# Kernel optimization log

Measured on AMD Instinct MI355X. Metric: run time of the kernel, lower is better.

Reference implementation:

```python
import jax, jax.numpy as jnp
import numpy as np

D_MODEL = 1024
D_INNER = 2048   # expand_factor * d_model
D_STATE = 16
D_CONV = 4
DT_RANK = 64     # ceil(d_model / 16)
EPS = 1e-5


def setup_inputs() -> dict:
    key = jax.random.key(0)
    ks = jax.random.split(key, 10)
    B, L = 2, 1024
    w = lambda k, shape, s: (jax.random.normal(k, shape, jnp.float32) * s)
    A = jnp.tile(jnp.arange(1, D_STATE + 1, dtype=jnp.float32), (D_INNER, 1))
    return {
        "hidden_states": jax.random.normal(ks[0], (B, L, D_MODEL), jnp.float32),
        "norm_w": jnp.ones((D_MODEL,), jnp.float32),
        "norm_b": jnp.zeros((D_MODEL,), jnp.float32),
        "in_proj_w": w(ks[1], (D_MODEL, 2 * D_INNER), 0.02),
        "conv_w": w(ks[2], (D_INNER, D_CONV), 0.2),
        "conv_b": jnp.zeros((D_INNER,), jnp.float32),
        "x_proj_w": w(ks[3], (D_INNER, DT_RANK + 2 * D_STATE), 0.02),
        "dt_proj_w": w(ks[4], (DT_RANK, D_INNER), 0.1),
        "dt_proj_b": w(ks[5], (D_INNER,), 0.1),
        "A_log": jnp.log(A),
        "D_param": jnp.ones((D_INNER,), jnp.float32),
        "out_proj_w": w(ks[6], (D_INNER, D_MODEL), 0.02),
    }


def _causal_depthwise_conv(x, conv_w, conv_b):
    # x: [B, L, d_inner] -> causal depthwise conv, kernel size D_CONV
    B, L, C = x.shape
    xt = jnp.transpose(x, (0, 2, 1))                 # [B, C, L]
    xt = jnp.pad(xt, ((0, 0), (0, 0), (D_CONV - 1, 0)))  # left pad == torch pad+truncate
    k = conv_w[:, None, :]                            # [C, 1, K] (OIH, groups=C)
    y = jax.lax.conv_general_dilated(
        xt, k, window_strides=(1,), padding="VALID",
        dimension_numbers=("NCH", "OIH", "NCH"), feature_group_count=C)
    y = y + conv_b[None, :, None]
    return jnp.transpose(y, (0, 2, 1))                # [B, L, C]


def _selective_scan(u, delta, A, Bm, Cm, D_param):
    # u, delta: [B, L, d_inner]; A: [d_inner, d_state]; Bm, Cm: [B, L, d_state]
    dA = jnp.exp(delta[..., None] * A[None, None])            # [B,L,d,n]
    dBu = delta[..., None] * Bm[:, :, None, :] * u[..., None]  # [B,L,d,n]
    h0 = jnp.zeros((u.shape[0], u.shape[2], A.shape[1]), u.dtype)

    def step(h, inp):
        dA_t, dBu_t, c_t = inp          # [B,d,n], [B,d,n], [B,n]
        h = dA_t * h + dBu_t
        y = jnp.einsum("bdn,bn->bd", h, c_t)
        return h, y

    xs = (jnp.moveaxis(dA, 1, 0), jnp.moveaxis(dBu, 1, 0), jnp.moveaxis(Cm, 1, 0))
    _, ys = jax.lax.scan(step, h0, xs)   # ys: [L, B, d]
    y = jnp.moveaxis(ys, 0, 1)           # [B, L, d]
    return y + u * D_param[None, None]


def reference(hidden_states, norm_w, norm_b, in_proj_w, conv_w, conv_b,
              x_proj_w, dt_proj_w, dt_proj_b, A_log, D_param, out_proj_w):
    h = hidden_states
    mu = jnp.mean(h, axis=-1, keepdims=True)
    var = jnp.mean(jnp.square(h - mu), axis=-1, keepdims=True)
    h = (h - mu) * jax.lax.rsqrt(var + EPS) * norm_w + norm_b

    xz = h @ in_proj_w                       # [B,L,2*d_inner]
    x, z = jnp.split(xz, 2, axis=-1)
    x = _causal_depthwise_conv(x, conv_w, conv_b)
    x = jax.nn.silu(x)

    A = -jnp.exp(A_log)                      # [d_inner, d_state]
    xp = x @ x_proj_w                        # [B,L,dt_rank+2*d_state]
    dt_r = xp[..., :DT_RANK]
    Bm = xp[..., DT_RANK:DT_RANK + D_STATE]
    Cm = xp[..., DT_RANK + D_STATE:]
    delta = jax.nn.softplus(dt_r @ dt_proj_w + dt_proj_b)  # [B,L,d_inner]

    y = _selective_scan(x, delta, A, Bm, Cm, D_param)
    y = y * jax.nn.silu(z)
    return y @ out_proj_w
```

## Files before the change

### kernel.cpp

```cpp
#include <hip/hip_runtime.h>
#include <hip/hip_bf16.h>

#define D_MODEL 1024
#define D_INNER 2048
#define D_STATE 16
#define DT_RANK 64
#define NB 2
#define LSEQ 1024
#define NROWS (NB * LSEQ)
#define XPN 96
#define NC 32
#define CL 32

typedef __attribute__((ext_vector_type(8))) short bf16x8;
typedef __attribute__((ext_vector_type(4))) float f32x4;

__device__ __forceinline__ unsigned short f2bf(float x) {
    __hip_bfloat16 h = __float2bfloat16(x);
    return *reinterpret_cast<unsigned short*>(&h);
}
__device__ __forceinline__ float bf2f(unsigned short u) {
    unsigned int v = ((unsigned int)u) << 16;
    float f;
    __builtin_memcpy(&f, &v, 4);
    return f;
}
__device__ __forceinline__ unsigned short f2h(float x) {
    _Float16 h = (_Float16)x;
    unsigned short u;
    __builtin_memcpy(&u, &h, 2);
    return u;
}
__device__ __forceinline__ float h2f(unsigned short u) {
    _Float16 h;
    __builtin_memcpy(&h, &u, 2);
    return (float)h;
}

__global__ __launch_bounds__(256) void ln_kernel(const float* __restrict__ x,
                                                 const float* __restrict__ w,
                                                 const float* __restrict__ bnorm,
                                                 unsigned short* __restrict__ outb) {
    int row = blockIdx.x;
    const float4* xr = (const float4*)(x + (size_t)row * D_MODEL);
    float4 v = xr[threadIdx.x];
    float s = v.x + v.y + v.z + v.w;
    float sq = v.x * v.x + v.y * v.y + v.z * v.z + v.w * v.w;
#pragma unroll
    for (int off = 32; off > 0; off >>= 1) {
        s += __shfl_down(s, off);
        sq += __shfl_down(sq, off);
    }
    __shared__ float ws[4], wq[4];
    __shared__ float smu, srstd;
    int wave = threadIdx.x >> 6;
    if ((threadIdx.x & 63) == 0) { ws[wave] = s; wq[wave] = sq; }
    __syncthreads();
    if (threadIdx.x == 0) {
        float ts = ws[0] + ws[1] + ws[2] + ws[3];
        float tq = wq[0] + wq[1] + wq[2] + wq[3];
        float mu = ts * (1.f / D_MODEL);
        float var = tq * (1.f / D_MODEL) - mu * mu;
        smu = mu;
        srstd = rsqrtf(var + 1e-5f);
    }
    __syncthreads();
    float mu = smu, rstd = srstd;
    float4 wv = ((const float4*)w)[threadIdx.x];
    float4 bv = ((const float4*)bnorm)[threadIdx.x];
    ushort4 pk;
    pk.x = f2bf((v.x - mu) * rstd * wv.x + bv.x);
    pk.y = f2bf((v.y - mu) * rstd * wv.y + bv.y);
    pk.z = f2bf((v.z - mu) * rstd * wv.z + bv.z);
    pk.w = f2bf((v.w - mu) * rstd * wv.w + bv.w);
    *(ushort4*)(outb + (size_t)row * D_MODEL + threadIdx.x * 4) = pk;
}

__global__ __launch_bounds__(256) void wcast_t(const float* __restrict__ W,
                                               unsigned short* __restrict__ Wt,
                                               int K, int Nreal, int Npad) {
    __shared__ float t[32][33];
    int tn = blockIdx.x * 32, tk = blockIdx.y * 32;
    for (int e = threadIdx.x; e < 1024; e += 256) {
        int r = e >> 5, c = e & 31;
        int n = tn + c;
        t[r][c] = (n < Nreal) ? W[(size_t)(tk + r) * Nreal + n] : 0.f;
    }
    __syncthreads();
    for (int e = threadIdx.x; e < 1024; e += 256) {
        int r = e >> 5, c = e & 31;
        Wt[(size_t)(tn + r) * K + tk + c] = f2bf(t[c][r]);
    }
}

template <int EPI>
__global__ __launch_bounds__(256) void gemm_bf16(const unsigned short* __restrict__ A,
                                                 const unsigned short* __restrict__ Bt,
                                                 const float* __restrict__ bias,
                                                 float* __restrict__ C,
                                                 void* __restrict__ C2,
                                                 int M, int K, int ldc, int Nreal) {
    __shared__ unsigned short As[128 * 32];
    __shared__ unsigned short Bs[128 * 32];
    int nwg = gridDim.x * gridDim.y;
    int orig = blockIdx.y * gridDim.x + blockIdx.x;
    int q = nwg >> 3, r = nwg & 7;
    int xcd = orig & 7, idx = orig >> 3;
    int newid = (xcd < r ? xcd * (q + 1) : r * (q + 1) + (xcd - r) * q) + idx;
    int bx = newid % gridDim.x, by = newid / gridDim.x;

    int tid = threadIdx.x;
    int lane = tid & 63;
    int wave = tid >> 6;
    int wr = (wave >> 1) * 64, wc = (wave & 1) * 64;
    int bm = by * 128, bn = bx * 128;
    int kchunk = K / gridDim.z;
    int kbeg = blockIdx.z * kchunk;

    f32x4 acc[4][4];
#pragma unroll
    for (int i = 0; i < 4; ++i)
#pragma unroll
        for (int j = 0; j < 4; ++j) acc[i][j] = (f32x4){0.f, 0.f, 0.f, 0.f};

    int r0 = tid >> 2;
    int c0 = (tid & 3) * 8;
    const unsigned short* a0 = A + (size_t)(bm + r0) * K + c0;
    const unsigned short* a1 = A + (size_t)(bm + 64 + r0) * K + c0;
    const unsigned short* b0 = Bt + (size_t)(bn + r0) * K + c0;
    const unsigned short* b1 = Bt + (size_t)(bn + 64 + r0) * K + c0;
    unsigned short* asw0 = As + (size_t)(tid & ~63) * 8;
    unsigned short* asw1 = As + 2048 + (size_t)(tid & ~63) * 8;
    unsigned short* bsw0 = Bs + (size_t)(tid & ~63) * 8;
    unsigned short* bsw1 = Bs + 2048 + (size_t)(tid & ~63) * 8;

    int ar = lane & 15;
    int ko = (lane >> 4) * 8;

    for (int k0 = kbeg; k0 < kbeg + kchunk; k0 += 32) {
        __syncthreads();
        __builtin_amdgcn_global_load_lds((const __attribute__((address_space(1))) void*)(a0 + k0),
                                         (__attribute__((address_space(3))) void*)asw0, 16, 0, 0);
        __builtin_amdgcn_global_load_lds((const __attribute__((address_space(1))) void*)(a1 + k0),
                                         (__attribute__((address_space(3))) void*)asw1, 16, 0, 0);
        __builtin_amdgcn_global_load_lds((const __attribute__((address_space(1))) void*)(b0 + k0),
                                         (__attribute__((address_space(3))) void*)bsw0, 16, 0, 0);
        __builtin_amdgcn_global_load_lds((const __attribute__((address_space(1))) void*)(b1 + k0),
                                         (__attribute__((address_space(3))) void*)bsw1, 16, 0, 0);
        __syncthreads();
        bf16x8 af[4], bfr[4];
#pragma unroll
        for (int i = 0; i < 4; ++i)
            af[i] = *(const bf16x8*)&As[(size_t)(wr + i * 16 + ar) * 32 + ko];
#pragma unroll
        for (int j = 0; j < 4; ++j)
            bfr[j] = *(const bf16x8*)&Bs[(size_t)(wc + j * 16 + ar) * 32 + ko];
#pragma unroll
        for (int i = 0; i < 4; ++i)
#pragma unroll
            for (int j = 0; j < 4; ++j)
                acc[i][j] = __builtin_amdgcn_mfma_f32_16x16x32_bf16(af[i], bfr[j], acc[i][j], 0, 0, 0);
    }

    int crow0 = bm + wr + (lane >> 4) * 4;
    int ccol0 = bn + wc + (lane & 15);
    size_t zoff = (size_t)blockIdx.z * (size_t)M * ldc;
#pragma unroll
    for (int i = 0; i < 4; ++i)
#pragma unroll
        for (int j = 0; j < 4; ++j) {
            int col = ccol0 + j * 16;
            if (EPI == 0) {
                if (col < Nreal) {
                    float* cp = C + zoff + (size_t)(crow0 + i * 16) * ldc + col;
#pragma unroll
                    for (int rr = 0; rr < 4; ++rr) cp[(size_t)rr * ldc] = acc[i][j][rr];
                }
            } else if (EPI == 1) {
                float bv = bias[col];
#pragma unroll
                for (int rr = 0; rr < 4; ++rr) {
                    float v = acc[i][j][rr] + bv;
                    v = (v > 20.f) ? v : log1pf(__expf(v));
                    C[(size_t)(crow0 + i * 16 + rr) * ldc + col] = v;
                }
            } else if (EPI == 2) {
                if (col < 2048) {
#pragma unroll
                    for (int rr = 0; rr < 4; ++rr)
                        C[(size_t)(crow0 + i * 16 + rr) * 2048 + col] = acc[i][j][rr];
                } else {
                    unsigned short* cz = (unsigned short*)C2;
#pragma unroll
                    for (int rr = 0; rr < 4; ++rr)
                        cz[(size_t)(crow0 + i * 16 + rr) * 2048 + (col - 2048)] = f2bf(acc[i][j][rr]);
                }
            } else {
                unsigned short* cp = (unsigned short*)C2 + zoff + (size_t)(crow0 + i * 16) * ldc + col;
#pragma unroll
                for (int rr = 0; rr < 4; ++rr) cp[(size_t)rr * ldc] = f2h(acc[i][j][rr]);
            }
        }
}

__global__ __launch_bounds__(256) void reduce_xp(const float* __restrict__ part,
                                                 float* __restrict__ xp,
                                                 unsigned short* __restrict__ dtr) {
    int t = blockIdx.x * 256 + threadIdx.x;
    float s = 0.f;
#pragma unroll
    for (int k = 0; k < 16; ++k) s += part[(size_t)k * (NROWS * XPN) + t];
    xp[t] = s;
    int row = t / 96, col = t - row * 96;
    if (col < 64) dtr[(size_t)row * 64 + col] = f2bf(s);
}

__global__ __launch_bounds__(256) void reduce_out(const unsigned short* __restrict__ part,
                                                  float* __restrict__ out) {
    int t = blockIdx.x * 256 + threadIdx.x;
    const size_t stride = (size_t)NROWS * D_MODEL;
    ushort4 p0 = ((const ushort4*)part)[t];
    ushort4 p1 = ((const ushort4*)(part + stride))[t];
    ushort4 p2 = ((const ushort4*)(part + 2 * stride))[t];
    ushort4 p3 = ((const ushort4*)(part + 3 * stride))[t];
    float4 o;
    o.x = h2f(p0.x) + h2f(p1.x) + h2f(p2.x) + h2f(p3.x);
    o.y = h2f(p0.y) + h2f(p1.y) + h2f(p2.y) + h2f(p3.y);
    o.z = h2f(p0.z) + h2f(p1.z) + h2f(p2.z) + h2f(p3.z);
    o.w = h2f(p0.w) + h2f(p1.w) + h2f(p2.w) + h2f(p3.w);
    ((float4*)out)[t] = o;
}

__global__ __launch_bounds__(256) void conv_silu_kernel(const float* __restrict__ xx,
                                                        const float* __restrict__ cw,
                                                        const float* __restrict__ cb,
                                                        unsigned short* __restrict__ outb) {
    int gid = blockIdx.x * 256 + threadIdx.x;
    int d4 = (gid & 511) << 2;
    int bl = gid >> 9;
    int l = bl & (LSEQ - 1);
    const float* base = xx + (size_t)bl * D_INNER + d4;
    float4 zr = make_float4(0.f, 0.f, 0.f, 0.f);
    float4 x0 = *(const float4*)base;
    float4 x1 = (l >= 1) ? *(const float4*)(base - D_INNER) : zr;
    float4 x2 = (l >= 2) ? *(const float4*)(base - 2 * D_INNER) : zr;
    float4 x3 = (l >= 3) ? *(const float4*)(base - 3 * D_INNER) : zr;
    float4 bias = *(const float4*)(cb + d4);
    const float4* wv = (const float4*)(cw + (size_t)d4 * 4);
    float xs0[4] = {x0.x, x0.y, x0.z, x0.w};
    float xs1[4] = {x1.x, x1.y, x1.z, x1.w};
    float xs2[4] = {x2.x, x2.y, x2.z, x2.w};
    float xs3[4] = {x3.x, x3.y, x3.z, x3.w};
    float bs[4] = {bias.x, bias.y, bias.z, bias.w};
    ushort4 ob;
    unsigned short* obp = (unsigned short*)&ob;
#pragma unroll
    for (int e = 0; e < 4; ++e) {
        float4 we = wv[e];
        float acc = bs[e];
        acc = fmaf(we.w, xs0[e], acc);
        acc = fmaf(we.z, xs1[e], acc);
        acc = fmaf(we.y, xs2[e], acc);
        acc = fmaf(we.x, xs3[e], acc);
        obp[e] = f2bf(acc / (1.f + __expf(-acc)));
    }
    *(ushort4*)(outb + (size_t)bl * D_INNER + d4) = ob;
}

__global__ __launch_bounds__(256) void scan_local(const float* __restrict__ xp,
                                                  const float* __restrict__ delta,
                                                  const unsigned short* __restrict__ ub,
                                                  const float* __restrict__ A_log,
                                                  float* __restrict__ hst,
                                                  float* __restrict__ sdel) {
    int bc = blockIdx.x >> 3;
    int b = bc >> 5, c = bc & (NC - 1);
    int d = (blockIdx.x & 7) * 256 + threadIdx.x;
    int base_r = b * LSEQ + c * CL;
    __shared__ float Bsm[CL * 16];
    for (int e = threadIdx.x; e < CL * 16; e += 256) {
        int l = e >> 4, n = e & 15;
        Bsm[e] = xp[(size_t)(base_r + l) * XPN + DT_RANK + n];
    }
    __syncthreads();
    float Av[16];
    const float4* ap = (const float4*)(A_log + (size_t)d * 16);
#pragma unroll
    for (int qq = 0; qq < 4; ++qq) {
        float4 a = ap[qq];
        Av[4 * qq + 0] = -__expf(a.x); Av[4 * qq + 1] = -__expf(a.y);
        Av[4 * qq + 2] = -__expf(a.z); Av[4 * qq + 3] = -__expf(a.w);
    }
    float h[16] = {};
    float sd = 0.f;
    const float* dp = delta + (size_t)base_r * D_INNER + d;
    const unsigned short* up = ub + (size_t)base_r * D_INNER + d;
#pragma unroll 4
    for (int l = 0; l < CL; ++l) {
        float dv = dp[(size_t)l * D_INNER];
        float u = bf2f(up[(size_t)l * D_INNER]);
        float du = dv * u;
        sd += dv;
#pragma unroll
        for (int n = 0; n < 16; ++n) {
            float dA = __expf(dv * Av[n]);
            h[n] = fmaf(dA, h[n], du * Bsm[l * 16 + n]);
        }
    }
    size_t hi = ((size_t)(c * NB + b) * D_INNER + d) * 16;
#pragma unroll
    for (int qq = 0; qq < 4; ++qq) {
        float4 v = make_float4(h[4 * qq], h[4 * qq + 1], h[4 * qq + 2], h[4 * qq + 3]);
        *(float4*)(hst + hi + 4 * qq) = v;
    }
    sdel[(size_t)(c * NB + b) * D_INNER + d] = sd;
}

__global__ __launch_bounds__(256) void scan_combine(const float* __restrict__ A_log,
                                                    const float* __restrict__ sdel,
                                                    float* __restrict__ hst) {
    int t = blockIdx.x * 256 + threadIdx.x;
    int n = t & 15, d = (t >> 4) & (D_INNER - 1), b = t >> 15;
    float Avn = -__expf(A_log[(size_t)d * 16 + n]);
    float h = 0.f;
#pragma unroll 4
    for (int c = 0; c < NC; ++c) {
        size_t base = (size_t)(c * NB + b) * D_INNER + d;
        float* hp = hst + base * 16 + n;
        float S = sdel[base];
        float tmp = *hp;
        *hp = h;
        h = fmaf(__expf(Avn * S), h, tmp);
    }
}

__global__ __launch_bounds__(256) void scan_final(const float* __restrict__ xp,
                                                  const float* __restrict__ dlt,
                                                  const unsigned short* __restrict__ ub,
                                                  const unsigned short* __restrict__ zb,
                                                  const float* __restrict__ hst,
                                                  const float* __restrict__ A_log,
                                                  const float* __restrict__ Dp,
                                                  unsigned short* __restrict__ yb) {
    int bc = blockIdx.x >> 3;
    int b = bc >> 5, c = bc & (NC - 1);
    int d = (blockIdx.x & 7) * 256 + threadIdx.x;
    int base_r = b * LSEQ + c * CL;
    __shared__ float Bsm[CL * 16], Csm[CL * 16];
    for (int e = threadIdx.x; e < CL * 16; e += 256) {
        int l = e >> 4, n = e & 15;
        Bsm[e] = xp[(size_t)(base_r + l) * XPN + DT_RANK + n];
        Csm[e] = xp[(size_t)(base_r + l) * XPN + DT_RANK + 16 + n];
    }
    __syncthreads();
    float Av[16];
    const float4* ap = (const float4*)(A_log + (size_t)d * 16);
#pragma unroll
    for (int qq = 0; qq < 4; ++qq) {
        float4 a = ap[qq];
        Av[4 * qq + 0] = -__expf(a.x); Av[4 * qq + 1] = -__expf(a.y);
        Av[4 * qq + 2] = -__expf(a.z); Av[4 * qq + 3] = -__expf(a.w);
    }
    float h[16];
    size_t hi = ((size_t)(c * NB + b) * D_INNER + d) * 16;
#pragma unroll
    for (int qq = 0; qq < 4; ++qq) {
        float4 v = *(const float4*)(hst + hi + 4 * qq);
        h[4 * qq] = v.x; h[4 * qq + 1] = v.y; h[4 * qq + 2] = v.z; h[4 * qq + 3] = v.w;
    }
    float Dv = Dp[d];
    const float* dyp = dlt + (size_t)base_r * D_INNER + d;
    const unsigned short* up = ub + (size_t)base_r * D_INNER + d;
    const unsigned short* zp = zb + (size_t)base_r * D_INNER + d;
#pragma unroll 4
    for (int l = 0; l < CL; ++l) {
        float dv = dyp[(size_t)l * D_INNER];
        float u = bf2f(up[(size_t)l * D_INNER]);
        float du = dv * u;
        float acc = 0.f;
#pragma unroll
        for (int n = 0; n < 16; ++n) {
            float dA = __expf(dv * Av[n]);
            h[n] = fmaf(dA, h[n], du * Bsm[l * 16 + n]);
            acc = fmaf(h[n], Csm[l * 16 + n], acc);
        }
        float yv = fmaf(u, Dv, acc);
        float zv = bf2f(zp[(size_t)l * D_INNER]);
        float sz = zv / (1.f + __expf(-zv));
        yb[(size_t)(base_r + l) * D_INNER + d] = f2bf(yv * sz);
    }
}

extern "C" void kernel_launch(void* const* d_in, const int* in_sizes, int n_in,
                              void* d_out, int out_size, void* d_ws, size_t ws_size,
                              hipStream_t stream) {
    const float* hidden = (const float*)d_in[0];
    const float* norm_w = (const float*)d_in[1];
    const float* norm_b = (const float*)d_in[2];
    const float* in_proj_w = (const float*)d_in[3];
    const float* conv_w = (const float*)d_in[4];
    const float* conv_b = (const float*)d_in[5];
    const float* x_proj_w = (const float*)d_in[6];
    const float* dt_proj_w = (const float*)d_in[7];
    const float* dt_proj_b = (const float*)d_in[8];
    const float* A_log = (const float*)d_in[9];
    const float* D_param = (const float*)d_in[10];
    const float* out_proj_w = (const float*)d_in[11];
    float* out = (float*)d_out;

    float* wsf = (float*)d_ws;
    unsigned short* hbufb = (unsigned short*)wsf;
    float* xpbuf = wsf;
    float* sdelbuf = wsf + 196608;
    unsigned short* dtrb = (unsigned short*)(wsf + 327680);
    unsigned short* wDt = (unsigned short*)(wsf + 458752);
    unsigned short* wOt = (unsigned short*)wsf;
    float* xzx = wsf + 1048576;
    unsigned short* xzz = (unsigned short*)(wsf + 5242880);
    unsigned short* xcb = (unsigned short*)(wsf + 7340032);
    unsigned short* yb = xcb;
    float* dltbuf = wsf + 9437184;
    unsigned short* wAt = (unsigned short*)dltbuf;
    float* xpart = dltbuf;
    unsigned short* wXt = (unsigned short*)(dltbuf + 3145728);
    float* hst = xzx;
    unsigned short* opart = (unsigned short*)xzx;

    wcast_t<<<dim3(4096 / 32, 1024 / 32), 256, 0, stream>>>(in_proj_w, wAt, 1024, 4096, 4096);
    wcast_t<<<dim3(128 / 32, 2048 / 32), 256, 0, stream>>>(x_proj_w, wXt, 2048, 96, 128);

    ln_kernel<<<NROWS, 256, 0, stream>>>(hidden, norm_w, norm_b, hbufb);

    gemm_bf16<2><<<dim3(4096 / 128, NROWS / 128, 1), 256, 0, stream>>>(
        hbufb, wAt, nullptr, xzx, xzz, NROWS, 1024, 2048, 4096);

    wcast_t<<<dim3(2048 / 32, 64 / 32), 256, 0, stream>>>(dt_proj_w, wDt, 64, 2048, 2048);

    conv_silu_kernel<<<(NROWS * D_INNER) / 1024, 256, 0, stream>>>(xzx, conv_w, conv_b, xcb);

    gemm_bf16<0><<<dim3(1, NROWS / 128, 16), 256, 0, stream>>>(
        xcb, wXt, nullptr, xpart, nullptr, NROWS, 2048, XPN, XPN);

    reduce_xp<<<(NROWS * XPN) / 256, 256, 0, stream>>>(xpart, xpbuf, dtrb);

    gemm_bf16<1><<<dim3(D_INNER / 128, NROWS / 128, 1), 256, 0, stream>>>(
        dtrb, wDt, dt_proj_b, dltbuf, nullptr, NROWS, 64, D_INNER, D_INNER);

    scan_local<<<NB * NC * (D_INNER / 256), 256, 0, stream>>>(
        xpbuf, dltbuf, xcb, A_log, hst, sdelbuf);
    scan_combine<<<(NB * D_INNER * D_STATE) / 256, 256, 0, stream>>>(
        A_log, sdelbuf, hst);
    scan_final<<<NB * NC * (D_INNER / 256), 256, 0, stream>>>(
        xpbuf, dltbuf, xcb, xzz, hst, A_log, D_param, yb);

    wcast_t<<<dim3(1024 / 32, 2048 / 32), 256, 0, stream>>>(out_proj_w, wOt, 2048, 1024, 1024);

    gemm_bf16<3><<<dim3(1024 / 128, NROWS / 128, 4), 256, 0, stream>>>(
        yb, wOt, nullptr, nullptr, opart, NROWS, 2048, 1024, 1024);

    reduce_out<<<(NROWS * D_MODEL / 4) / 256, 256, 0, stream>>>(opart, out);
}
```

Measured before the change: 200.6 us.

## Fuse dt_proj into xp reduction, merge weight casts, store x and delta as bf16

The three weight transpose-casts are merged into one launch, and the dt_proj weight cast is dropped. The xp partial-sum reduction now also performs the small dt_proj matmul in fp32 on CUDA cores, followed by the softplus, which removes a separate GEMM launch and the dtr buffer. The x half of in_proj and the delta tensor are stored as bf16 instead of fp32, which cuts memory traffic in the conv, scan_local and scan_final kernels. The cost is lower precision for x and delta, and a per-block CUDA-core matmul that re-reads dt_proj_w from global memory.

```diff
diff --git a/kernel.cpp b/kernel.cpp
--- a/kernel.cpp
+++ b/kernel.cpp
@@ -11,6 +11,7 @@
 #define XPN 96
 #define NC 32
 #define CL 32
+#define DR_ROWS 8
 
 typedef __attribute__((ext_vector_type(8))) short bf16x8;
 typedef __attribute__((ext_vector_type(4))) float f32x4;
@@ -76,11 +77,18 @@
     *(ushort4*)(outb + (size_t)row * D_MODEL + threadIdx.x * 4) = pk;
 }
 
-__global__ __launch_bounds__(256) void wcast_t(const float* __restrict__ W,
-                                               unsigned short* __restrict__ Wt,
-                                               int K, int Nreal, int Npad) {
+__global__ __launch_bounds__(256) void wcast_all(const float* __restrict__ W0, unsigned short* __restrict__ D0,
+                                                 const float* __restrict__ W1, unsigned short* __restrict__ D1,
+                                                 const float* __restrict__ W2, unsigned short* __restrict__ D2) {
+    int bid = blockIdx.x;
+    const float* W;
+    unsigned short* Dst;
+    int K, Nreal, bx, by;
+    if (bid < 4096) { W = W0; Dst = D0; K = 1024; Nreal = 4096; bx = bid & 127; by = bid >> 7; }
+    else if (bid < 4352) { int j = bid - 4096; W = W1; Dst = D1; K = 2048; Nreal = 96; bx = j & 3; by = j >> 2; }
+    else { int j = bid - 4352; W = W2; Dst = D2; K = 2048; Nreal = 1024; bx = j & 31; by = j >> 5; }
     __shared__ float t[32][33];
-    int tn = blockIdx.x * 32, tk = blockIdx.y * 32;
+    int tn = bx * 32, tk = by * 32;
     for (int e = threadIdx.x; e < 1024; e += 256) {
         int r = e >> 5, c = e & 31;
         int n = tn + c;
@@ -89,14 +97,13 @@
     __syncthreads();
     for (int e = threadIdx.x; e < 1024; e += 256) {
         int r = e >> 5, c = e & 31;
-        Wt[(size_t)(tn + r) * K + tk + c] = f2bf(t[c][r]);
+        Dst[(size_t)(tn + r) * K + tk + c] = f2bf(t[c][r]);
     }
 }
 
 template <int EPI>
 __global__ __launch_bounds__(256) void gemm_bf16(const unsigned short* __restrict__ A,
                                                  const unsigned short* __restrict__ Bt,
-                                                 const float* __restrict__ bias,
                                                  float* __restrict__ C,
                                                  void* __restrict__ C2,
                                                  int M, int K, int ldc, int Nreal) {
@@ -176,21 +183,14 @@
 #pragma unroll
                     for (int rr = 0; rr < 4; ++rr) cp[(size_t)rr * ldc] = acc[i][j][rr];
                 }
-            } else if (EPI == 1) {
-                float bv = bias[col];
-#pragma unroll
-                for (int rr = 0; rr < 4; ++rr) {
-                    float v = acc[i][j][rr] + bv;
-                    v = (v > 20.f) ? v : log1pf(__expf(v));
-                    C[(size_t)(crow0 + i * 16 + rr) * ldc + col] = v;
-                }
             } else if (EPI == 2) {
+                unsigned short* cx = (unsigned short*)C;
+                unsigned short* cz = (unsigned short*)C2;
                 if (col < 2048) {
 #pragma unroll
                     for (int rr = 0; rr < 4; ++rr)
-                        C[(size_t)(crow0 + i * 16 + rr) * 2048 + col] = acc[i][j][rr];
+                        cx[(size_t)(crow0 + i * 16 + rr) * 2048 + col] = f2bf(acc[i][j][rr]);
                 } else {
-                    unsigned short* cz = (unsigned short*)C2;
 #pragma unroll
                     for (int rr = 0; rr < 4; ++rr)
                         cz[(size_t)(crow0 + i * 16 + rr) * 2048 + (col - 2048)] = f2bf(acc[i][j][rr]);
@@ -203,16 +203,55 @@
         }
 }
 
-__global__ __launch_bounds__(256) void reduce_xp(const float* __restrict__ part,
-                                                 float* __restrict__ xp,
-                                                 unsigned short* __restrict__ dtr) {
-    int t = blockIdx.x * 256 + threadIdx.x;
-    float s = 0.f;
-#pragma unroll
-    for (int k = 0; k < 16; ++k) s += part[(size_t)k * (NROWS * XPN) + t];
-    xp[t] = s;
-    int row = t / 96, col = t - row * 96;
-    if (col < 64) dtr[(size_t)row * 64 + col] = f2bf(s);
+__global__ __launch_bounds__(256) void reduce_delta(const float* __restrict__ part,
+                                                    const float* __restrict__ Wdt,
+                                                    const float* __restrict__ dtb,
+                                                    float* __restrict__ xp,
+                                                    unsigned short* __restrict__ delta) {
+    int r0 = blockIdx.x * DR_ROWS;
+    __shared__ float dtr[DR_ROWS][64];
+    for (int idx = threadIdx.x; idx < DR_ROWS * XPN; idx += 256) {
+        int rr = idx / XPN, cc = idx - rr * XPN;
+        size_t off = (size_t)(r0 + rr) * XPN + cc;
+        float s = 0.f;
+#pragma unroll
+        for (int p = 0; p < 16; ++p) s += part[(size_t)p * ((size_t)NROWS * XPN) + off];
+        xp[off] = s;
+        if (cc < 64) dtr[rr][cc] = s;
+    }
+    __syncthreads();
+    int c0 = threadIdx.x * 8;
+    float acc[DR_ROWS][8] = {};
+    for (int k = 0; k < 64; ++k) {
+        float4 w0 = *(const float4*)(Wdt + (size_t)k * D_INNER + c0);
+        float4 w1 = *(const float4*)(Wdt + (size_t)k * D_INNER + c0 + 4);
+        float wv[8] = {w0.x, w0.y, w0.z, w0.w, w1.x, w1.y, w1.z, w1.w};
+#pragma unroll
+        for (int rr = 0; rr < DR_ROWS; ++rr) {
+            float s = dtr[rr][k];
+#pragma unroll
+            for (int j = 0; j < 8; ++j) acc[rr][j] = fmaf(s, wv[j], acc[rr][j]);
+        }
+    }
+    float4 b0 = *(const float4*)(dtb + c0);
+    float4 b1 = *(const float4*)(dtb + c0 + 4);
+    float bias[8] = {b0.x, b0.y, b0.z, b0.w, b1.x, b1.y, b1.z, b1.w};
+#pragma unroll
+    for (int rr = 0; rr < DR_ROWS; ++rr) {
+        ushort4 o0, o1;
+        unsigned short tmp[8];
+#pragma unroll
+        for (int j = 0; j < 8; ++j) {
+            float v = acc[rr][j] + bias[j];
+            v = (v > 20.f) ? v : log1pf(__expf(v));
+            tmp[j] = f2bf(v);
+        }
+        o0.x = tmp[0]; o0.y = tmp[1]; o0.z = tmp[2]; o0.w = tmp[3];
+        o1.x = tmp[4]; o1.y = tmp[5]; o1.z = tmp[6]; o1.w = tmp[7];
+        unsigned short* dp = delta + (size_t)(r0 + rr) * D_INNER + c0;
+        *(ushort4*)dp = o0;
+        *(ushort4*)(dp + 4) = o1;
+    }
 }
 
 __global__ __launch_bounds__(256) void reduce_out(const unsigned short* __restrict__ part,
@@ -231,7 +270,7 @@
     ((float4*)out)[t] = o;
 }
 
-__global__ __launch_bounds__(256) void conv_silu_kernel(const float* __restrict__ xx,
+__global__ __launch_bounds__(256) void conv_silu_kernel(const unsigned short* __restrict__ xx,
                                                         const float* __restrict__ cw,
                                                         const float* __restrict__ cb,
                                                         unsigned short* __restrict__ outb) {
@@ -239,18 +278,18 @@
     int d4 = (gid & 511) << 2;
     int bl = gid >> 9;
     int l = bl & (LSEQ - 1);
-    const float* base = xx + (size_t)bl * D_INNER + d4;
-    float4 zr = make_float4(0.f, 0.f, 0.f, 0.f);
-    float4 x0 = *(const float4*)base;
-    float4 x1 = (l >= 1) ? *(const float4*)(base - D_INNER) : zr;
-    float4 x2 = (l >= 2) ? *(const float4*)(base - 2 * D_INNER) : zr;
-    float4 x3 = (l >= 3) ? *(const float4*)(base - 3 * D_INNER) : zr;
+    const unsigned short* base = xx + (size_t)bl * D_INNER + d4;
+    ushort4 zr4 = {0, 0, 0, 0};
+    ushort4 X0 = *(const ushort4*)base;
+    ushort4 X1 = (l >= 1) ? *(const ushort4*)(base - D_INNER) : zr4;
+    ushort4 X2 = (l >= 2) ? *(const ushort4*)(base - 2 * D_INNER) : zr4;
+    ushort4 X3 = (l >= 3) ? *(const ushort4*)(base - 3 * D_INNER) : zr4;
     float4 bias = *(const float4*)(cb + d4);
     const float4* wv = (const float4*)(cw + (size_t)d4 * 4);
-    float xs0[4] = {x0.x, x0.y, x0.z, x0.w};
-    float xs1[4] = {x1.x, x1.y, x1.z, x1.w};
-    float xs2[4] = {x2.x, x2.y, x2.z, x2.w};
-    float xs3[4] = {x3.x, x3.y, x3.z, x3.w};
+    float xs0[4] = {bf2f(X0.x), bf2f(X0.y), bf2f(X0.z), bf2f(X0.w)};
+    float xs1[4] = {bf2f(X1.x), bf2f(X1.y), bf2f(X1.z), bf2f(X1.w)};
+    float xs2[4] = {bf2f(X2.x), bf2f(X2.y), bf2f(X2.z), bf2f(X2.w)};
+    float xs3[4] = {bf2f(X3.x), bf2f(X3.y), bf2f(X3.z), bf2f(X3.w)};
     float bs[4] = {bias.x, bias.y, bias.z, bias.w};
     ushort4 ob;
     unsigned short* obp = (unsigned short*)&ob;
@@ -268,7 +307,7 @@
 }
 
 __global__ __launch_bounds__(256) void scan_local(const float* __restrict__ xp,
-                                                  const float* __restrict__ delta,
+                                                  const unsigned short* __restrict__ delta,
                                                   const unsigned short* __restrict__ ub,
                                                   const float* __restrict__ A_log,
                                                   float* __restrict__ hst,
@@ -293,11 +332,11 @@
     }
     float h[16] = {};
     float sd = 0.f;
-    const float* dp = delta + (size_t)base_r * D_INNER + d;
+    const unsigned short* dp = delta + (size_t)base_r * D_INNER + d;
     const unsigned short* up = ub + (size_t)base_r * D_INNER + d;
 #pragma unroll 4
     for (int l = 0; l < CL; ++l) {
-        float dv = dp[(size_t)l * D_INNER];
+        float dv = bf2f(dp[(size_t)l * D_INNER]);
         float u = bf2f(up[(size_t)l * D_INNER]);
         float du = dv * u;
         sd += dv;
@@ -335,7 +374,7 @@
 }
 
 __global__ __launch_bounds__(256) void scan_final(const float* __restrict__ xp,
-                                                  const float* __restrict__ dlt,
+                                                  const unsigned short* __restrict__ delta,
                                                   const unsigned short* __restrict__ ub,
                                                   const unsigned short* __restrict__ zb,
                                                   const float* __restrict__ hst,
@@ -369,12 +408,12 @@
         h[4 * qq] = v.x; h[4 * qq + 1] = v.y; h[4 * qq + 2] = v.z; h[4 * qq + 3] = v.w;
     }
     float Dv = Dp[d];
-    const float* dyp = dlt + (size_t)base_r * D_INNER + d;
+    const unsigned short* dp = delta + (size_t)base_r * D_INNER + d;
     const unsigned short* up = ub + (size_t)base_r * D_INNER + d;
     const unsigned short* zp = zb + (size_t)base_r * D_INNER + d;
 #pragma unroll 4
     for (int l = 0; l < CL; ++l) {
-        float dv = dyp[(size_t)l * D_INNER];
+        float dv = bf2f(dp[(size_t)l * D_INNER]);
         float u = bf2f(up[(size_t)l * D_INNER]);
         float du = dv * u;
         float acc = 0.f;
@@ -412,51 +451,41 @@
     unsigned short* hbufb = (unsigned short*)wsf;
     float* xpbuf = wsf;
     float* sdelbuf = wsf + 196608;
-    unsigned short* dtrb = (unsigned short*)(wsf + 327680);
-    unsigned short* wDt = (unsigned short*)(wsf + 458752);
-    unsigned short* wOt = (unsigned short*)wsf;
-    float* xzx = wsf + 1048576;
-    unsigned short* xzz = (unsigned short*)(wsf + 5242880);
-    unsigned short* xcb = (unsigned short*)(wsf + 7340032);
-    unsigned short* yb = xcb;
-    float* dltbuf = wsf + 9437184;
-    unsigned short* wAt = (unsigned short*)dltbuf;
-    float* xpart = dltbuf;
-    unsigned short* wXt = (unsigned short*)(dltbuf + 3145728);
-    float* hst = xzx;
-    unsigned short* opart = (unsigned short*)xzx;
-
-    wcast_t<<<dim3(4096 / 32, 1024 / 32), 256, 0, stream>>>(in_proj_w, wAt, 1024, 4096, 4096);
-    wcast_t<<<dim3(128 / 32, 2048 / 32), 256, 0, stream>>>(x_proj_w, wXt, 2048, 96, 128);
+    unsigned short* xb = (unsigned short*)(wsf + 1048576);
+    float* hst = wsf + 1048576;
+    unsigned short* zb = (unsigned short*)(wsf + 3145728);
+    unsigned short* ub = (unsigned short*)(wsf + 5242880);
+    unsigned short* yb = ub;
+    unsigned short* wAt = (unsigned short*)(wsf + 7340032);
+    float* xpart = wsf + 7340032;
+    unsigned short* opart = (unsigned short*)(wsf + 7340032);
+    unsigned short* wXt = (unsigned short*)(wsf + 10485760);
+    unsigned short* deltab = (unsigned short*)(wsf + 11665408);
+    unsigned short* wOt = (unsigned short*)(wsf + 13762560);
+
+    wcast_all<<<6400, 256, 0, stream>>>(in_proj_w, wAt, x_proj_w, wXt, out_proj_w, wOt);
 
     ln_kernel<<<NROWS, 256, 0, stream>>>(hidden, norm_w, norm_b, hbufb);
 
     gemm_bf16<2><<<dim3(4096 / 128, NROWS / 128, 1), 256, 0, stream>>>(
-        hbufb, wAt, nullptr, xzx, xzz, NROWS, 1024, 2048, 4096);
-
-    wcast_t<<<dim3(2048 / 32, 64 / 32), 256, 0, stream>>>(dt_proj_w, wDt, 64, 2048, 2048);
-
-    conv_silu_kernel<<<(NROWS * D_INNER) / 1024, 256, 0, stream>>>(xzx, conv_w, conv_b, xcb);
+        hbufb, wAt, (float*)xb, zb, NROWS, 1024, 2048, 4096);
+
+    conv_silu_kernel<<<(NROWS * D_INNER) / 1024, 256, 0, stream>>>(xb, conv_w, conv_b, ub);
 
     gemm_bf16<0><<<dim3(1, NROWS / 128, 16), 256, 0, stream>>>(
-        xcb, wXt, nullptr, xpart, nullptr, NROWS, 2048, XPN, XPN);
-
-    reduce_xp<<<(NROWS * XPN) / 256, 256, 0, stream>>>(xpart, xpbuf, dtrb);
-
-    gemm_bf16<1><<<dim3(D_INNER / 128, NROWS / 128, 1), 256, 0, stream>>>(
-        dtrb, wDt, dt_proj_b, dltbuf, nullptr, NROWS, 64, D_INNER, D_INNER);
+        ub, wXt, xpart, nullptr, NROWS, 2048, XPN, XPN);
+
+    reduce_delta<<<NROWS / DR_ROWS, 256, 0, stream>>>(xpart, dt_proj_w, dt_proj_b, xpbuf, deltab);
 
     scan_local<<<NB * NC * (D_INNER / 256), 256, 0, stream>>>(
-        xpbuf, dltbuf, xcb, A_log, hst, sdelbuf);
+        xpbuf, deltab, ub, A_log, hst, sdelbuf);
     scan_combine<<<(NB * D_INNER * D_STATE) / 256, 256, 0, stream>>>(
         A_log, sdelbuf, hst);
     scan_final<<<NB * NC * (D_INNER / 256), 256, 0, stream>>>(
-        xpbuf, dltbuf, xcb, xzz, hst, A_log, D_param, yb);
-
-    wcast_t<<<dim3(1024 / 32, 2048 / 32), 256, 0, stream>>>(out_proj_w, wOt, 2048, 1024, 1024);
+        xpbuf, deltab, ub, zb, hst, A_log, D_param, yb);
 
     gemm_bf16<3><<<dim3(1024 / 128, NROWS / 128, 4), 256, 0, stream>>>(
-        yb, wOt, nullptr, nullptr, opart, NROWS, 2048, 1024, 1024);
+        yb, wOt, nullptr, opart, NROWS, 2048, 1024, 1024);
 
     reduce_out<<<(NROWS * D_MODEL / 4) / 256, 256, 0, stream>>>(opart, out);
 }
```

New measurement: 193.9 us. 3.4% less time.
